# Optimization experiments

Measured on AMD Instinct MI355X. Metric: run time of the kernel, lower is better.

The kernel has to match this reference:

```python
import jax, jax.numpy as jnp
import numpy as np

D_MODEL = 1024
N_HEADS = 16
D_Q = D_MODEL // N_HEADS
NEG = float(-2**32 + 1)


def setup_inputs() -> dict:
    key = jax.random.key(0)
    ks = jax.random.split(key, 8)
    B, L = 8, 1024
    q = jax.random.normal(ks[0], (B, L, D_MODEL), dtype=jnp.float32)
    k = jax.random.normal(ks[1], (B, L, D_MODEL), dtype=jnp.float32)
    # causal subsequent mask: 1 above the diagonal (positions to be masked)
    subseq_mask = jnp.broadcast_to(
        jnp.triu(jnp.ones((L, L), dtype=jnp.int32), k=1), (B, L, L))
    s = 1.0 / np.sqrt(D_MODEL)
    Wq = jax.random.normal(ks[2], (D_MODEL, D_MODEL), dtype=jnp.float32) * s
    Wk = jax.random.normal(ks[3], (D_MODEL, D_MODEL), dtype=jnp.float32) * s
    Wv = jax.random.normal(ks[4], (D_MODEL, D_MODEL), dtype=jnp.float32) * s
    bq = jax.random.normal(ks[5], (D_MODEL,), dtype=jnp.float32) * 0.01
    bk = jax.random.normal(ks[6], (D_MODEL,), dtype=jnp.float32) * 0.01
    bv = jax.random.normal(ks[7], (D_MODEL,), dtype=jnp.float32) * 0.01
    return {"q": q, "k": k, "subseq_mask": subseq_mask,
            "Wq": Wq, "bq": bq, "Wk": Wk, "bk": bk, "Wv": Wv, "bv": bv}


def reference(q, k, subseq_mask, Wq, bq, Wk, bk, Wv, bv):
    B, Lq, _ = q.shape
    Lk = k.shape[1]
    residual = q
    # projections; heads laid out as (H, B, L, d_q) matching torch permute(2,0,1,3)
    qp = (q @ Wq + bq).reshape(B, Lq, N_HEADS, D_Q).transpose(2, 0, 1, 3)
    kp = (k @ Wk + bk).reshape(B, Lk, N_HEADS, D_Q).transpose(2, 0, 1, 3)
    vp = (k @ Wv + bv).reshape(B, Lk, N_HEADS, D_Q).transpose(2, 0, 1, 3)
    # scaled scores: (H, B, Lq, Lk)
    scores = jnp.einsum('hbqd,hbkd->hbqk', qp, kp) / np.sqrt(D_Q)
    # key mask from PROJECTED k (faithful to source)
    key_masks = jnp.sign(jnp.abs(jnp.sum(kp, -1)))          # (H, B, Lk)
    scores = jnp.where(key_masks[:, :, None, :] == 0, NEG, scores)
    # subsequence (causal) mask, replicated over heads
    scores = jnp.where(subseq_mask[None, :, :, :] == 1, NEG, scores)
    attn = jax.nn.softmax(scores, axis=-1)
    # post-softmax query mask from PROJECTED q (faithful to source)
    query_masks = jnp.sign(jnp.abs(jnp.sum(qp, -1)))        # (H, B, Lq)
    attn = attn * query_masks[:, :, :, None]
    # dropout is identity in eval/reference mode
    out = jnp.einsum('hbqk,hbkd->hbqd', attn, vp)           # (H, B, Lq, d_q)
    out = out.transpose(1, 2, 0, 3).reshape(B, Lq, N_HEADS * D_Q)
    return out + residual
```

## Files before the change

kernel.cpp:

```cpp
#include <hip/hip_runtime.h>
#include <cstdint>
#include <cstddef>

#define DM 1024
#define NH 16
#define DQ 64
#define NB 8
#define LSEQ 1024

typedef __attribute__((ext_vector_type(8))) short short8;
typedef __attribute__((ext_vector_type(4))) float floatx4;

__device__ __forceinline__ unsigned short f2bf(float f) {
  union { float f; unsigned u; } v; v.f = f;
  unsigned r = v.u + 0x7FFFu + ((v.u >> 16) & 1u);
  return (unsigned short)(r >> 16);
}
__device__ __forceinline__ unsigned cvt_pk_bf16(float a, float b) {
  unsigned r;
  asm("v_cvt_pk_bf16_f32 %0, %1, %2" : "=v"(r) : "v"(a), "v"(b));
  return r;
}
__device__ __forceinline__ unsigned short f2bf_fast(float f) {
  unsigned r;
  asm("v_cvt_pk_bf16_f32 %0, %1, %1" : "=v"(r) : "v"(f));
  return (unsigned short)r;
}

__device__ __forceinline__ void async_load16(const void* g, void* l) {
  __builtin_amdgcn_global_load_lds(
      (const __attribute__((address_space(1))) unsigned int*)g,
      (__attribute__((address_space(3))) unsigned int*)l, 16, 0, 0);
}

__global__ __launch_bounds__(256) void prep(
    const float* __restrict__ q, const float* __restrict__ k,
    unsigned short* __restrict__ qb, unsigned short* __restrict__ kb,
    const float* __restrict__ Wq, const float* __restrict__ Wk,
    const float* __restrict__ Wv, unsigned short* __restrict__ Wt) {
  __shared__ float tile[32][33];
  const int bid = blockIdx.x;
  const int tid = threadIdx.x;
  if (bid < 8192) {
    size_t i = ((size_t)bid * 256 + tid) * 4;
    float4 a = *(const float4*)&q[i];
    uint2 r;
    r.x = cvt_pk_bf16(a.x, a.y);
    r.y = cvt_pk_bf16(a.z, a.w);
    *(uint2*)&qb[i] = r;
    float4 b = *(const float4*)&k[i];
    uint2 s;
    s.x = cvt_pk_bf16(b.x, b.y);
    s.y = cvt_pk_bf16(b.z, b.w);
    *(uint2*)&kb[i] = s;
  } else {
    const int t = bid - 8192;
    const int z = t >> 10;
    const int rr = t & 1023;
    const float* W = (z == 0) ? Wq : (z == 1) ? Wk : Wv;
    const int n0 = (rr & 31) * 32, k0 = (rr >> 5) * 32;
    const int tx = tid & 31, ty = tid >> 5;
    for (int j = ty; j < 32; j += 8)
      tile[j][tx] = W[(size_t)(k0 + j) * DM + n0 + tx];
    __syncthreads();
    unsigned short* o = Wt + (size_t)z * DM * DM;
    for (int j = ty; j < 32; j += 8)
      o[(size_t)(n0 + j) * DM + k0 + tx] = f2bf_fast(tile[tx][j]);
  }
}

__global__ __launch_bounds__(256, 4) void gemm_proj(
    const unsigned short* __restrict__ qb, const unsigned short* __restrict__ kb,
    const unsigned short* __restrict__ Wt,
    const float* __restrict__ bq, const float* __restrict__ bk, const float* __restrict__ bv,
    const float* __restrict__ ,
    unsigned short* __restrict__ Pq, unsigned short* __restrict__ Pk,
    unsigned short* __restrict__ Pvt,
    float* __restrict__ qmask, float* __restrict__ kmask) {
  const int z = blockIdx.z;
  const unsigned short* A = (z == 0) ? qb : kb;
  const unsigned short* Bt = Wt + (size_t)z * DM * DM;
  const float* bias = (z == 0) ? bq : (z == 1) ? bk : bv;

  __shared__ unsigned short smem[16384];
  unsigned short* As = smem;
  unsigned short* Bs = smem + 8192;

  const int tid = threadIdx.x;
  const int lane = tid & 63;
  const int wave = tid >> 6;
  const int l16 = lane & 15, quad = lane >> 4;
  const int wm = wave & 1, wn = wave >> 1;
  const int rowBase = blockIdx.x * 128;
  const int colBase = blockIdx.y * 128;

  floatx4 acc[4][4];
  const floatx4 zf = {0.f, 0.f, 0.f, 0.f};
#pragma unroll
  for (int i = 0; i < 4; i++)
#pragma unroll
    for (int j = 0; j < 4; j++) acc[i][j] = zf;

  const int srl = lane >> 3;
  const int sl7 = lane & 7;

  for (int kt = 0; kt < DM; kt += 64) {
#pragma unroll
    for (int cc = wave; cc < 16; cc += 4) {
      const int rl = cc * 8 + srl;
      const int ck = (sl7 ^ (rl & 7)) * 8;
      async_load16(A + (size_t)(rowBase + rl) * DM + kt + ck, &As[cc * 512]);
      async_load16(Bt + (size_t)(colBase + rl) * DM + kt + ck, &Bs[cc * 512]);
    }
    __syncthreads();

#pragma unroll
    for (int c = 0; c < 2; c++) {
      const int chnk = ((c << 2) + quad) ^ (l16 & 7);
      short8 af[4], bfr[4];
#pragma unroll
      for (int i = 0; i < 4; i++)
        af[i] = *(const short8*)&As[(wm * 64 + i * 16 + l16) * 64 + chnk * 8];
#pragma unroll
      for (int j = 0; j < 4; j++)
        bfr[j] = *(const short8*)&Bs[(wn * 64 + j * 16 + l16) * 64 + chnk * 8];
#pragma unroll
      for (int i = 0; i < 4; i++)
#pragma unroll
        for (int j = 0; j < 4; j++)
          acc[i][j] = __builtin_amdgcn_mfma_f32_16x16x32_bf16(af[i], bfr[j], acc[i][j], 0, 0, 0);
    }
    __syncthreads();
  }

#pragma unroll
  for (int j = 0; j < 4; j++) {
    const float bj = bias[colBase + wn * 64 + j * 16 + l16];
#pragma unroll
    for (int i = 0; i < 4; i++)
#pragma unroll
      for (int r = 0; r < 4; r++) acc[i][j][r] += bj;
  }

  if (z < 2) {
    float* mask = (z == 0) ? qmask : kmask;
    const int h = (colBase >> 6) + wn;
#pragma unroll
    for (int i = 0; i < 4; i++)
#pragma unroll
      for (int r = 0; r < 4; r++) {
        float rs = acc[i][0][r] + acc[i][1][r] + acc[i][2][r] + acc[i][3][r];
        rs += __shfl_xor(rs, 1);
        rs += __shfl_xor(rs, 2);
        rs += __shfl_xor(rs, 4);
        rs += __shfl_xor(rs, 8);
        if (l16 == 0) {
          const int row = rowBase + wm * 64 + i * 16 + quad * 4 + r;
          mask[((size_t)((row >> 10) * NH + h)) * LSEQ + (row & 1023)] = (rs != 0.f) ? 1.f : 0.f;
        }
      }
    unsigned short* P = (z == 0) ? Pq : Pk;
    const float pscale = (z == 0) ? 0.125f : 1.0f;
    const int bb2 = rowBase >> 10;
    const int l0 = (rowBase & 1023) + wm * 64;
    const size_t pbase = ((size_t)(bb2 * NH + h) * LSEQ + l0) * DQ;
    unsigned short* lds = smem + wave * 2304;
#pragma unroll
    for (int pass = 0; pass < 2; ++pass) {
#pragma unroll
      for (int ii = 0; ii < 2; ++ii) {
        const int i = pass * 2 + ii;
#pragma unroll
        for (int j = 0; j < 4; ++j)
#pragma unroll
          for (int r = 0; r < 4; ++r)
            lds[(ii * 16 + quad * 4 + r) * 72 + j * 16 + l16] = f2bf_fast(acc[i][j][r] * pscale);
      }
      asm volatile("s_waitcnt lgkmcnt(0)" ::: "memory");
#pragma unroll
      for (int ll = 0; ll < 4; ++ll) {
        const int c = ll * 8 + (lane >> 3);
        const int seg = lane & 7;
        int4 v = *(const int4*)&lds[c * 72 + seg * 8];
        *(int4*)&P[pbase + (size_t)(pass * 32 + c) * DQ + seg * 8] = v;
      }
      if (pass == 0) asm volatile("s_waitcnt lgkmcnt(0)" ::: "memory");
    }
  } else {
    const int b = rowBase >> 10;
    const int l0r = rowBase & 1023;
#pragma unroll
    for (int j = 0; j < 4; j++) {
      __syncthreads();
#pragma unroll
      for (int i = 0; i < 4; i++) {
        uint2 v;
        v.x = cvt_pk_bf16(acc[i][j][0], acc[i][j][1]);
        v.y = cvt_pk_bf16(acc[i][j][2], acc[i][j][3]);
        *(uint2*)&smem[(wn * 16 + l16) * 136 + wm * 64 + i * 16 + quad * 4] = v;
      }
      __syncthreads();
      const int c = tid >> 3, seg = tid & 7;
      const int col = colBase + (c >> 4) * 64 + j * 16 + (c & 15);
      const int hh = col >> 6, d = col & 63;
      int4 t0 = *(const int4*)&smem[c * 136 + seg * 16];
      int4 t1 = *(const int4*)&smem[c * 136 + seg * 16 + 8];
      const size_t g = ((size_t)((b * NH + hh) * DQ + d)) * LSEQ + l0r + seg * 16;
      *(int4*)&Pvt[g] = t0;
      *(int4*)&Pvt[g + 8] = t1;
    }
  }
}

__global__ __launch_bounds__(256, 4) void attn_kernel(
    const unsigned short* __restrict__ Q, const unsigned short* __restrict__ K,
    const unsigned short* __restrict__ Vt,
    const float* __restrict__ kmask, const float* __restrict__ qmask,
    const float* __restrict__ qin, float* __restrict__ out) {
  const int bh = blockIdx.x;
  const int qblk = 7 - blockIdx.y;
  const int b = bh >> 4, h = bh & 15;
  const size_t base = (size_t)bh * LSEQ * DQ;

  const int tid = threadIdx.x;
  const int lane = tid & 63;
  const int wave = tid >> 6;
  const int l16 = lane & 15, quad = lane >> 4;
  const int qw = qblk * 128 + wave * 32;

  __shared__ unsigned short Ks[2 * 4096];
  __shared__ unsigned short Vs[2 * 4096];
  __shared__ unsigned short Ps[4][2304];

  short8 qf[2][2];
#pragma unroll
  for (int sub = 0; sub < 2; sub++)
#pragma unroll
    for (int c = 0; c < 2; c++)
      qf[sub][c] = *(const short8*)&Q[base + (size_t)(qw + sub * 16 + l16) * DQ + c * 32 + quad * 8];

  const floatx4 zf = {0.f, 0.f, 0.f, 0.f};
  floatx4 o[2][4];
#pragma unroll
  for (int sub = 0; sub < 2; sub++)
#pragma unroll
    for (int jj = 0; jj < 4; jj++) o[sub][jj] = zf;
  float l_p[2][4] = {{0.f, 0.f, 0.f, 0.f}, {0.f, 0.f, 0.f, 0.f}};

  const int swz = (quad ^ (l16 & 7)) * 8;
  const int swz2 = ((quad + 4) ^ (l16 & 7)) * 8;
  const int vswz = (quad ^ (l16 >> 1)) * 8;
  const int vswz2 = ((quad + 4) ^ (l16 >> 1)) * 8;

  const int srl = (lane >> 3);
  const int ktiles = (qblk + 1) * 2;
  const int tmax = 2 * qblk + (wave >> 1);

  {
#pragma unroll
    for (int cc = wave; cc < 8; cc += 4) {
      const int rl = cc * 8 + srl;
      const int ck = ((lane & 7) ^ (rl & 7)) * 8;
      async_load16(&K[base + (size_t)rl * DQ + ck], &Ks[cc * 512]);
      const int cv = ((lane & 7) ^ ((rl >> 1) & 7)) * 8;
      async_load16(&Vt[base + (size_t)rl * LSEQ + cv], &Vs[cc * 512]);
    }
  }
  __syncthreads();

  for (int t = 0; t < ktiles; t++) {
    const int cur = t & 1;
    const int kt = t * 64;
    const bool live = (t <= tmax);

    float km[4];
    if (live) {
#pragma unroll
      for (int ct = 0; ct < 4; ct++) km[ct] = kmask[(size_t)bh * LSEQ + kt + ct * 16 + l16];
    }

    if (t + 1 < ktiles) {
      const int nkt = kt + 64;
      const int nb = (cur ^ 1) * 4096;
#pragma unroll
      for (int cc = wave; cc < 8; cc += 4) {
        const int rl = cc * 8 + srl;
        const int ck = ((lane & 7) ^ (rl & 7)) * 8;
        async_load16(&K[base + (size_t)(nkt + rl) * DQ + ck], &Ks[nb + cc * 512]);
        const int cv = ((lane & 7) ^ ((rl >> 1) & 7)) * 8;
        async_load16(&Vt[base + (size_t)rl * LSEQ + nkt + cv], &Vs[nb + cc * 512]);
      }
    }

    if (live) {
      const unsigned short* Kb = &Ks[cur * 4096];
      const unsigned short* Vb = &Vs[cur * 4096];
      const bool diag = (t == tmax);

#pragma unroll
      for (int sub = 0; sub < 2; sub++) {
        floatx4 s[4];
        __builtin_amdgcn_s_setprio(1);
#pragma unroll
        for (int ct = 0; ct < 4; ct++) {
          const int kr = (ct * 16 + l16) * 64;
          const short8 kf0 = *(const short8*)&Kb[kr + swz];
          const short8 kf1 = *(const short8*)&Kb[kr + swz2];
          floatx4 sv = zf;
          sv = __builtin_amdgcn_mfma_f32_16x16x32_bf16(qf[sub][0], kf0, sv, 0, 0, 0);
          sv = __builtin_amdgcn_mfma_f32_16x16x32_bf16(qf[sub][1], kf1, sv, 0, 0, 0);
          s[ct] = sv;
        }
        __builtin_amdgcn_s_setprio(0);
        const int row0 = qw + sub * 16 + quad * 4;
        unsigned short* pw = &Ps[wave][(sub * 16 + quad * 4) * 72];
        if (diag) {
#pragma unroll
          for (int ct = 0; ct < 4; ct++) {
            const int col = kt + ct * 16 + l16;
#pragma unroll
            for (int r = 0; r < 4; r++) {
              float e = __expf(s[ct][r]) * km[ct];
              e = (col <= row0 + r) ? e : 0.f;
              l_p[sub][r] += e;
              pw[r * 72 + ct * 16 + l16] = f2bf_fast(e);
            }
          }
        } else {
#pragma unroll
          for (int ct = 0; ct < 4; ct++) {
#pragma unroll
            for (int r = 0; r < 4; r++) {
              float e = __expf(s[ct][r]) * km[ct];
              l_p[sub][r] += e;
              pw[r * 72 + ct * 16 + l16] = f2bf_fast(e);
            }
          }
        }
      }

      short8 vf0[4], vf1[4];
#pragma unroll
      for (int jj = 0; jj < 4; jj++) {
        const int vr = (jj * 16 + l16) * 64;
        vf0[jj] = *(const short8*)&Vb[vr + vswz];
        vf1[jj] = *(const short8*)&Vb[vr + vswz2];
      }
      asm volatile("s_waitcnt lgkmcnt(0)" ::: "memory");

      short8 pf[2][2];
#pragma unroll
      for (int sub = 0; sub < 2; sub++) {
        pf[sub][0] = *(const short8*)&Ps[wave][(sub * 16 + l16) * 72 + quad * 8];
        pf[sub][1] = *(const short8*)&Ps[wave][(sub * 16 + l16) * 72 + 32 + quad * 8];
      }
      __builtin_amdgcn_s_setprio(1);
#pragma unroll
      for (int jj = 0; jj < 4; jj++) {
#pragma unroll
        for (int sub = 0; sub < 2; sub++) {
          o[sub][jj] = __builtin_amdgcn_mfma_f32_16x16x32_bf16(pf[sub][0], vf0[jj], o[sub][jj], 0, 0, 0);
          o[sub][jj] = __builtin_amdgcn_mfma_f32_16x16x32_bf16(pf[sub][1], vf1[jj], o[sub][jj], 0, 0, 0);
        }
      }
      __builtin_amdgcn_s_setprio(0);
    }
    __syncthreads();
  }

  const int hd = h * DQ;
#pragma unroll
  for (int sub = 0; sub < 2; sub++)
#pragma unroll
    for (int r = 0; r < 4; r++) {
      float lv = l_p[sub][r];
      lv += __shfl_xor(lv, 1);
      lv += __shfl_xor(lv, 2);
      lv += __shfl_xor(lv, 4);
      lv += __shfl_xor(lv, 8);
      const int row = qw + sub * 16 + quad * 4 + r;
      const float inv = qmask[(size_t)bh * LSEQ + row] / lv;
#pragma unroll
      for (int jj = 0; jj < 4; jj++) {
        const size_t oi = ((size_t)(b * LSEQ + row)) * DM + hd + jj * 16 + l16;
        out[oi] = o[sub][jj][r] * inv + qin[oi];
      }
    }
}

extern "C" void kernel_launch(void* const* d_in, const int* in_sizes, int n_in,
                              void* d_out, int out_size, void* d_ws, size_t ws_size,
                              hipStream_t stream) {
  const float* q = (const float*)d_in[0];
  const float* k = (const float*)d_in[1];
  const float* Wq = (const float*)d_in[3];
  const float* bq = (const float*)d_in[4];
  const float* Wk = (const float*)d_in[5];
  const float* bk = (const float*)d_in[6];
  const float* Wv = (const float*)d_in[7];
  const float* bv = (const float*)d_in[8];
  float* out = (float*)d_out;

  char* w = (char*)d_ws;
  unsigned short* qb = (unsigned short*)(w + 0);
  unsigned short* kb = (unsigned short*)(w + 16777216);
  unsigned short* Wt = (unsigned short*)(w + 33554432);
  unsigned short* Pq = (unsigned short*)(w + 39845888);
  unsigned short* Pk = (unsigned short*)(w + 56623104);
  unsigned short* Pvt = (unsigned short*)(w + 73400320);
  float* qmask = (float*)(w + 90177536);
  float* kmask = (float*)(w + 90701824);

  prep<<<8192 + 3072, 256, 0, stream>>>(q, k, qb, kb, Wq, Wk, Wv, Wt);
  gemm_proj<<<dim3(64, 8, 3), 256, 0, stream>>>(qb, kb, Wt, bq, bk, bv, nullptr,
                                                Pq, Pk, Pvt, qmask, kmask);
  attn_kernel<<<dim3(128, 8), 256, 0, stream>>>(Pq, Pk, Pvt, kmask, qmask, q, out);
}
```

Baseline: 247.9 us.

## Pair complementary causal query blocks per workgroup to balance work and share K/V

Each attention workgroup now handles two query blocks, qA and 7-qA, so every block does the same total amount of causal work. The K/V tiles loaded once into LDS serve both query blocks, which halves the number of K/V tile loads and halves the grid. The cost is a larger register footprint for the extra Q fragments and accumulators, so launch bounds drop from 4 to 3 blocks per CU. The grid also shrinks to 512 workgroups, which may lower parallelism on the GPU.

```diff
diff --git a/kernel.cpp b/kernel.cpp
--- a/kernel.cpp
+++ b/kernel.cpp
@@ -11,11 +11,6 @@
 typedef __attribute__((ext_vector_type(8))) short short8;
 typedef __attribute__((ext_vector_type(4))) float floatx4;
 
-__device__ __forceinline__ unsigned short f2bf(float f) {
-  union { float f; unsigned u; } v; v.f = f;
-  unsigned r = v.u + 0x7FFFu + ((v.u >> 16) & 1u);
-  return (unsigned short)(r >> 16);
-}
 __device__ __forceinline__ unsigned cvt_pk_bf16(float a, float b) {
   unsigned r;
   asm("v_cvt_pk_bf16_f32 %0, %1, %2" : "=v"(r) : "v"(a), "v"(b));
@@ -212,13 +207,14 @@
   }
 }
 
-__global__ __launch_bounds__(256, 4) void attn_kernel(
+__global__ __launch_bounds__(256, 3) void attn_kernel(
     const unsigned short* __restrict__ Q, const unsigned short* __restrict__ K,
     const unsigned short* __restrict__ Vt,
     const float* __restrict__ kmask, const float* __restrict__ qmask,
     const float* __restrict__ qin, float* __restrict__ out) {
   const int bh = blockIdx.x;
-  const int qblk = 7 - blockIdx.y;
+  const int qA = blockIdx.y;
+  const int qB = 7 - blockIdx.y;
   const int b = bh >> 4, h = bh & 15;
   const size_t base = (size_t)bh * LSEQ * DQ;
 
@@ -226,26 +222,30 @@
   const int lane = tid & 63;
   const int wave = tid >> 6;
   const int l16 = lane & 15, quad = lane >> 4;
-  const int qw = qblk * 128 + wave * 32;
+  const int qwA = qA * 128 + wave * 32;
+  const int qwB = qB * 128 + wave * 32;
 
   __shared__ unsigned short Ks[2 * 4096];
   __shared__ unsigned short Vs[2 * 4096];
   __shared__ unsigned short Ps[4][2304];
 
-  short8 qf[2][2];
+  short8 qfA[2][2], qfB[2][2];
 #pragma unroll
   for (int sub = 0; sub < 2; sub++)
 #pragma unroll
-    for (int c = 0; c < 2; c++)
-      qf[sub][c] = *(const short8*)&Q[base + (size_t)(qw + sub * 16 + l16) * DQ + c * 32 + quad * 8];
+    for (int c = 0; c < 2; c++) {
+      qfA[sub][c] = *(const short8*)&Q[base + (size_t)(qwA + sub * 16 + l16) * DQ + c * 32 + quad * 8];
+      qfB[sub][c] = *(const short8*)&Q[base + (size_t)(qwB + sub * 16 + l16) * DQ + c * 32 + quad * 8];
+    }
 
   const floatx4 zf = {0.f, 0.f, 0.f, 0.f};
-  floatx4 o[2][4];
+  floatx4 oA[2][4], oB[2][4];
 #pragma unroll
   for (int sub = 0; sub < 2; sub++)
 #pragma unroll
-    for (int jj = 0; jj < 4; jj++) o[sub][jj] = zf;
-  float l_p[2][4] = {{0.f, 0.f, 0.f, 0.f}, {0.f, 0.f, 0.f, 0.f}};
+    for (int jj = 0; jj < 4; jj++) { oA[sub][jj] = zf; oB[sub][jj] = zf; }
+  float lA[2][4] = {{0.f, 0.f, 0.f, 0.f}, {0.f, 0.f, 0.f, 0.f}};
+  float lB[2][4] = {{0.f, 0.f, 0.f, 0.f}, {0.f, 0.f, 0.f, 0.f}};
 
   const int swz = (quad ^ (l16 & 7)) * 8;
   const int swz2 = ((quad + 4) ^ (l16 & 7)) * 8;
@@ -253,8 +253,9 @@
   const int vswz2 = ((quad + 4) ^ (l16 >> 1)) * 8;
 
   const int srl = (lane >> 3);
-  const int ktiles = (qblk + 1) * 2;
-  const int tmax = 2 * qblk + (wave >> 1);
+  const int ktiles = (qB + 1) * 2;
+  const int tmaxA = 2 * qA + (wave >> 1);
+  const int tmaxB = 2 * qB + (wave >> 1);
 
   {
 #pragma unroll
@@ -271,10 +272,11 @@
   for (int t = 0; t < ktiles; t++) {
     const int cur = t & 1;
     const int kt = t * 64;
-    const bool live = (t <= tmax);
+    const bool liveB = (t <= tmaxB);
+    const bool liveA = (t <= tmaxA);
 
     float km[4];
-    if (live) {
+    if (liveB) {
 #pragma unroll
       for (int ct = 0; ct < 4; ct++) km[ct] = kmask[(size_t)bh * LSEQ + kt + ct * 16 + l16];
     }
@@ -292,78 +294,140 @@
       }
     }
 
-    if (live) {
+    if (liveB) {
       const unsigned short* Kb = &Ks[cur * 4096];
       const unsigned short* Vb = &Vs[cur * 4096];
-      const bool diag = (t == tmax);
-
-#pragma unroll
-      for (int sub = 0; sub < 2; sub++) {
-        floatx4 s[4];
+
+      {
+        const bool diag = (t == tmaxB);
+#pragma unroll
+        for (int sub = 0; sub < 2; sub++) {
+          floatx4 s[4];
+          __builtin_amdgcn_s_setprio(1);
+#pragma unroll
+          for (int ct = 0; ct < 4; ct++) {
+            const int kr = (ct * 16 + l16) * 64;
+            const short8 kf0 = *(const short8*)&Kb[kr + swz];
+            const short8 kf1 = *(const short8*)&Kb[kr + swz2];
+            floatx4 sv = zf;
+            sv = __builtin_amdgcn_mfma_f32_16x16x32_bf16(qfB[sub][0], kf0, sv, 0, 0, 0);
+            sv = __builtin_amdgcn_mfma_f32_16x16x32_bf16(qfB[sub][1], kf1, sv, 0, 0, 0);
+            s[ct] = sv;
+          }
+          __builtin_amdgcn_s_setprio(0);
+          const int row0 = qwB + sub * 16 + quad * 4;
+          unsigned short* pw = &Ps[wave][(sub * 16 + quad * 4) * 72];
+          if (diag) {
+#pragma unroll
+            for (int ct = 0; ct < 4; ct++) {
+              const int col = kt + ct * 16 + l16;
+#pragma unroll
+              for (int r = 0; r < 4; r++) {
+                float e = __expf(s[ct][r]) * km[ct];
+                e = (col <= row0 + r) ? e : 0.f;
+                lB[sub][r] += e;
+                pw[r * 72 + ct * 16 + l16] = f2bf_fast(e);
+              }
+            }
+          } else {
+#pragma unroll
+            for (int ct = 0; ct < 4; ct++) {
+#pragma unroll
+              for (int r = 0; r < 4; r++) {
+                float e = __expf(s[ct][r]) * km[ct];
+                lB[sub][r] += e;
+                pw[r * 72 + ct * 16 + l16] = f2bf_fast(e);
+              }
+            }
+          }
+        }
+        asm volatile("s_waitcnt lgkmcnt(0)" ::: "memory");
+        short8 pf[2][2];
+#pragma unroll
+        for (int sub = 0; sub < 2; sub++) {
+          pf[sub][0] = *(const short8*)&Ps[wave][(sub * 16 + l16) * 72 + quad * 8];
+          pf[sub][1] = *(const short8*)&Ps[wave][(sub * 16 + l16) * 72 + 32 + quad * 8];
+        }
         __builtin_amdgcn_s_setprio(1);
 #pragma unroll
-        for (int ct = 0; ct < 4; ct++) {
-          const int kr = (ct * 16 + l16) * 64;
-          const short8 kf0 = *(const short8*)&Kb[kr + swz];
-          const short8 kf1 = *(const short8*)&Kb[kr + swz2];
-          floatx4 sv = zf;
-          sv = __builtin_amdgcn_mfma_f32_16x16x32_bf16(qf[sub][0], kf0, sv, 0, 0, 0);
-          sv = __builtin_amdgcn_mfma_f32_16x16x32_bf16(qf[sub][1], kf1, sv, 0, 0, 0);
-          s[ct] = sv;
+        for (int jj = 0; jj < 4; jj++) {
+          const int vr = (jj * 16 + l16) * 64;
+          const short8 vf0 = *(const short8*)&Vb[vr + vswz];
+          const short8 vf1 = *(const short8*)&Vb[vr + vswz2];
+#pragma unroll
+          for (int sub = 0; sub < 2; sub++) {
+            oB[sub][jj] = __builtin_amdgcn_mfma_f32_16x16x32_bf16(pf[sub][0], vf0, oB[sub][jj], 0, 0, 0);
+            oB[sub][jj] = __builtin_amdgcn_mfma_f32_16x16x32_bf16(pf[sub][1], vf1, oB[sub][jj], 0, 0, 0);
+          }
         }
         __builtin_amdgcn_s_setprio(0);
-        const int row0 = qw + sub * 16 + quad * 4;
-        unsigned short* pw = &Ps[wave][(sub * 16 + quad * 4) * 72];
-        if (diag) {
+      }
+
+      if (liveA) {
+        asm volatile("s_waitcnt lgkmcnt(0)" ::: "memory");
+        const bool diag = (t == tmaxA);
+#pragma unroll
+        for (int sub = 0; sub < 2; sub++) {
+          floatx4 s[4];
+          __builtin_amdgcn_s_setprio(1);
 #pragma unroll
           for (int ct = 0; ct < 4; ct++) {
-            const int col = kt + ct * 16 + l16;
-#pragma unroll
-            for (int r = 0; r < 4; r++) {
-              float e = __expf(s[ct][r]) * km[ct];
-              e = (col <= row0 + r) ? e : 0.f;
-              l_p[sub][r] += e;
-              pw[r * 72 + ct * 16 + l16] = f2bf_fast(e);
+            const int kr = (ct * 16 + l16) * 64;
+            const short8 kf0 = *(const short8*)&Kb[kr + swz];
+            const short8 kf1 = *(const short8*)&Kb[kr + swz2];
+            floatx4 sv = zf;
+            sv = __builtin_amdgcn_mfma_f32_16x16x32_bf16(qfA[sub][0], kf0, sv, 0, 0, 0);
+            sv = __builtin_amdgcn_mfma_f32_16x16x32_bf16(qfA[sub][1], kf1, sv, 0, 0, 0);
+            s[ct] = sv;
+          }
+          __builtin_amdgcn_s_setprio(0);
+          const int row0 = qwA + sub * 16 + quad * 4;
+          unsigned short* pw = &Ps[wave][(sub * 16 + quad * 4) * 72];
+          if (diag) {
+#pragma unroll
+            for (int ct = 0; ct < 4; ct++) {
+              const int col = kt + ct * 16 + l16;
+#pragma unroll
+              for (int r = 0; r < 4; r++) {
+                float e = __expf(s[ct][r]) * km[ct];
+                e = (col <= row0 + r) ? e : 0.f;
+                lA[sub][r] += e;
+                pw[r * 72 + ct * 16 + l16] = f2bf_fast(e);
+              }
             }
-          }
-        } else {
-#pragma unroll
-          for (int ct = 0; ct < 4; ct++) {
-#pragma unroll
-            for (int r = 0; r < 4; r++) {
-              float e = __expf(s[ct][r]) * km[ct];
-              l_p[sub][r] += e;
-              pw[r * 72 + ct * 16 + l16] = f2bf_fast(e);
+          } else {
+#pragma unroll
+            for (int ct = 0; ct < 4; ct++) {
+#pragma unroll
+              for (int r = 0; r < 4; r++) {
+                float e = __expf(s[ct][r]) * km[ct];
+                lA[sub][r] += e;
+                pw[r * 72 + ct * 16 + l16] = f2bf_fast(e);
+              }
             }
           }
         }
-      }
-
-      short8 vf0[4], vf1[4];
-#pragma unroll
-      for (int jj = 0; jj < 4; jj++) {
-        const int vr = (jj * 16 + l16) * 64;
-        vf0[jj] = *(const short8*)&Vb[vr + vswz];
-        vf1[jj] = *(const short8*)&Vb[vr + vswz2];
-      }
-      asm volatile("s_waitcnt lgkmcnt(0)" ::: "memory");
-
-      short8 pf[2][2];
-#pragma unroll
-      for (int sub = 0; sub < 2; sub++) {
-        pf[sub][0] = *(const short8*)&Ps[wave][(sub * 16 + l16) * 72 + quad * 8];
-        pf[sub][1] = *(const short8*)&Ps[wave][(sub * 16 + l16) * 72 + 32 + quad * 8];
-      }
-      __builtin_amdgcn_s_setprio(1);
-#pragma unroll
-      for (int jj = 0; jj < 4; jj++) {
+        asm volatile("s_waitcnt lgkmcnt(0)" ::: "memory");
+        short8 pf[2][2];
 #pragma unroll
         for (int sub = 0; sub < 2; sub++) {
-          o[sub][jj] = __builtin_amdgcn_mfma_f32_16x16x32_bf16(pf[sub][0], vf0[jj], o[sub][jj], 0, 0, 0);
-          o[sub][jj] = __builtin_amdgcn_mfma_f32_16x16x32_bf16(pf[sub][1], vf1[jj], o[sub][jj], 0, 0, 0);
-        }
-      }
-      __builtin_amdgcn_s_setprio(0);
+          pf[sub][0] = *(const short8*)&Ps[wave][(sub * 16 + l16) * 72 + quad * 8];
+          pf[sub][1] = *(const short8*)&Ps[wave][(sub * 16 + l16) * 72 + 32 + quad * 8];
+        }
+        __builtin_amdgcn_s_setprio(1);
+#pragma unroll
+        for (int jj = 0; jj < 4; jj++) {
+          const int vr = (jj * 16 + l16) * 64;
+          const short8 vf0 = *(const short8*)&Vb[vr + vswz];
+          const short8 vf1 = *(const short8*)&Vb[vr + vswz2];
+#pragma unroll
+          for (int sub = 0; sub < 2; sub++) {
+            oA[sub][jj] = __builtin_amdgcn_mfma_f32_16x16x32_bf16(pf[sub][0], vf0, oA[sub][jj], 0, 0, 0);
+            oA[sub][jj] = __builtin_amdgcn_mfma_f32_16x16x32_bf16(pf[sub][1], vf1, oA[sub][jj], 0, 0, 0);
+          }
+        }
+        __builtin_amdgcn_s_setprio(0);
+      }
     }
     __syncthreads();
   }
@@ -373,17 +437,34 @@
   for (int sub = 0; sub < 2; sub++)
 #pragma unroll
     for (int r = 0; r < 4; r++) {
-      float lv = l_p[sub][r];
+      float lv = lB[sub][r];
       lv += __shfl_xor(lv, 1);
       lv += __shfl_xor(lv, 2);
       lv += __shfl_xor(lv, 4);
       lv += __shfl_xor(lv, 8);
-      const int row = qw + sub * 16 + quad * 4 + r;
+      const int row = qwB + sub * 16 + quad * 4 + r;
       const float inv = qmask[(size_t)bh * LSEQ + row] / lv;
 #pragma unroll
       for (int jj = 0; jj < 4; jj++) {
         const size_t oi = ((size_t)(b * LSEQ + row)) * DM + hd + jj * 16 + l16;
-        out[oi] = o[sub][jj][r] * inv + qin[oi];
+        out[oi] = oB[sub][jj][r] * inv + qin[oi];
+      }
+    }
+#pragma unroll
+  for (int sub = 0; sub < 2; sub++)
+#pragma unroll
+    for (int r = 0; r < 4; r++) {
+      float lv = lA[sub][r];
+      lv += __shfl_xor(lv, 1);
+      lv += __shfl_xor(lv, 2);
+      lv += __shfl_xor(lv, 4);
+      lv += __shfl_xor(lv, 8);
+      const int row = qwA + sub * 16 + quad * 4 + r;
+      const float inv = qmask[(size_t)bh * LSEQ + row] / lv;
+#pragma unroll
+      for (int jj = 0; jj < 4; jj++) {
+        const size_t oi = ((size_t)(b * LSEQ + row)) * DM + hd + jj * 16 + l16;
+        out[oi] = oA[sub][jj][r] * inv + qin[oi];
       }
     }
 }
@@ -414,5 +495,5 @@
   prep<<<8192 + 3072, 256, 0, stream>>>(q, k, qb, kb, Wq, Wk, Wv, Wt);
   gemm_proj<<<dim3(64, 8, 3), 256, 0, stream>>>(qb, kb, Wt, bq, bk, bv, nullptr,
                                                 Pq, Pk, Pvt, qmask, kmask);
-  attn_kernel<<<dim3(128, 8), 256, 0, stream>>>(Pq, Pk, Pvt, kmask, qmask, q, out);
-}
+  attn_kernel<<<dim3(128, 4), 256, 0, stream>>>(Pq, Pk, Pvt, kmask, qmask, q, out);
+}
```

Measured after the change: 268.1 us. 8.2% more time.
